# Optimization experiments

Measured on AMD Instinct MI355X. Metric: run time of the kernel, lower is better.

Reference implementation:

```python
import jax, jax.numpy as jnp
import numpy as np


def gru_step(x, h, Wih, Whh, bih, bhh):
    gi = x @ Wih.T + bih            # [N, 3H]
    gh = h @ Whh.T + bhh            # [N, 3H]
    ir, iz, inn = jnp.split(gi, 3, axis=-1)
    hr, hz, hn = jnp.split(gh, 3, axis=-1)
    r = jax.nn.sigmoid(ir + hr)
    z = jax.nn.sigmoid(iz + hz)
    n = jnp.tanh(inn + r * hn)
    return (1.0 - z) * n + z * h


def setup_inputs() -> dict:
    key = jax.random.key(0)
    ks = jax.random.split(key, 24)
    B, T, X, HE, HC = 8192, 30, 64, 256, 32
    s = 0.05
    rn = lambda k, shp: (jax.random.normal(k, shp, dtype=jnp.float32) * s)
    return {
        "batch_features": jax.random.normal(ks[0], (B, 2, T, X), dtype=jnp.float32),
        "coords": jax.random.uniform(ks[1], (B, T, 4), dtype=jnp.float32) * 100.0,
        "valid_mask": jax.random.bernoulli(ks[2], 0.8, (B, T)),
        # Event GRU (2 layers, input 64, hidden 256)
        "Wih0": rn(ks[3], (3 * HE, X)),  "Whh0": rn(ks[4], (3 * HE, HE)),
        "bih0": jnp.zeros((3 * HE,), jnp.float32), "bhh0": jnp.zeros((3 * HE,), jnp.float32),
        "Wih1": rn(ks[5], (3 * HE, HE)), "Whh1": rn(ks[6], (3 * HE, HE)),
        "bih1": jnp.zeros((3 * HE,), jnp.float32), "bhh1": jnp.zeros((3 * HE,), jnp.float32),
        # Coord GRU (1 layer, input 4, hidden 32)
        "WihC": rn(ks[7], (3 * HC, 4)), "WhhC": rn(ks[8], (3 * HC, HC)),
        "bihC": jnp.zeros((3 * HC,), jnp.float32), "bhhC": jnp.zeros((3 * HC,), jnp.float32),
        # Fusion module
        "We": rn(ks[9], (128, HE)), "be": jnp.zeros((128,), jnp.float32),
        "Wc": rn(ks[10], (128, HC)), "bc": jnp.zeros((128,), jnp.float32),
        "W1": rn(ks[11], (128, 256)), "b1": jnp.zeros((128,), jnp.float32),
        "W2": rn(ks[12], (2, 128)), "b2": jnp.zeros((2,), jnp.float32),
    }


def reference(batch_features, coords, valid_mask,
              Wih0, Whh0, bih0, bhh0, Wih1, Whh1, bih1, bhh1,
              WihC, WhhC, bihC, bhhC,
              We, be, Wc, bc, W1, b1, W2, b2):
    B, F, T, X = batch_features.shape  # F == 2 frames
    N = B * T
    HE = Whh0.shape[1]
    HC = WhhC.shape[1]
    # [B,2,T,X] -> [N,2,X]: per-track (prev, curr) feature sequence
    feats = jnp.transpose(batch_features, (0, 2, 1, 3)).reshape(N, F, X)
    h0 = jnp.zeros((N, HE), batch_features.dtype)
    h1 = jnp.zeros((N, HE), batch_features.dtype)
    for t in range(F):  # fixed 2-step unroll (n_frames=2)
        h0 = gru_step(feats[:, t], h0, Wih0, Whh0, bih0, bhh0)
        h1 = gru_step(h0, h1, Wih1, Whh1, bih1, bhh1)
    event_out = h1  # [N, 256] (dropout between GRU layers inactive in eval)
    # coord GRU: single step from zero state
    c = coords.reshape(N, 4)
    coord_out = gru_step(c, jnp.zeros((N, HC), coords.dtype), WihC, WhhC, bihC, bhhC)
    # fusion
    ep = event_out @ We.T + be          # [N,128]
    cp = coord_out @ Wc.T + bc          # [N,128]
    hid = jax.nn.relu(jnp.concatenate([ep, cp], axis=-1) @ W1.T + b1)
    logits = hid @ W2.T + b2            # [N,2]
    logits = logits.reshape(B, T, 2)
    # invalid tracks were skipped in the original; mask them to zero here
    return jnp.where(valid_mask[..., None], logits, 0.0)
```

## Files before the change

### kernel.cpp

```cpp
#include <hip/hip_runtime.h>


#define NROWS 245760
#define TT 30
#define KC 64

typedef __attribute__((ext_vector_type(4))) float f32x4;
typedef __attribute__((ext_vector_type(8))) short bf16x8;
typedef __attribute__((ext_vector_type(4))) int i32x4;

__device__ __forceinline__ float bf2f(unsigned short u) {
    union { unsigned int u; float f; } v; v.u = ((unsigned int)u) << 16; return v.f;
}
__device__ __forceinline__ unsigned short f2bf(float f) {
    union { float f; unsigned int u; } v; v.f = f;
    unsigned int u = v.u;
    unsigned int r = u + 0x7fffu + ((u >> 16) & 1u);
    return (unsigned short)(r >> 16);
}
__device__ __forceinline__ float fexp2c(float x) {
    return __builtin_amdgcn_exp2f(fminf(x, 80.f));
}
__device__ __forceinline__ float fsigmoid(float x) {
    return __builtin_amdgcn_rcpf(1.f + fexp2c(-1.44269504f * x));
}
__device__ __forceinline__ float ftanh(float x) {
    float t = fexp2c(-2.88539008f * x);
    return (1.f - t) * __builtin_amdgcn_rcpf(1.f + t);
}
__device__ __forceinline__ f32x4 mfma16(bf16x8 a, bf16x8 b, f32x4 c) {
    return __builtin_amdgcn_mfma_f32_16x16x32_bf16(a, b, c, 0, 0, 0);
}


__global__ void cvt_bf16(const float* __restrict__ src, unsigned short* __restrict__ dst, int n) {
    int i = blockIdx.x * 256 + threadIdx.x;
    if (i < n) dst[i] = f2bf(src[i]);
}

__global__ void bias_prep(const float* __restrict__ bih0, const float* __restrict__ bhh0, float* __restrict__ BC0,
                          const float* __restrict__ bih1, const float* __restrict__ bhh1, float* __restrict__ BC1) {
    int j = threadIdx.x;
    BC0[j]       = bih0[j]       + bhh0[j];
    BC0[256 + j] = bih0[256 + j] + bhh0[256 + j];
    BC0[512 + j] = bih0[512 + j];
    BC0[768 + j] = bhh0[512 + j];
    BC1[j]       = bih1[j]       + bhh1[j];
    BC1[256 + j] = bih1[256 + j] + bhh1[256 + j];
    BC1[512 + j] = bih1[512 + j];
    BC1[768 + j] = bhh1[512 + j];
}

__global__ void fuse_prep(const float* __restrict__ We, const float* __restrict__ be,
                          const float* __restrict__ Wc, const float* __restrict__ bc_,
                          const float* __restrict__ W1, const float* __restrict__ b1,
                          unsigned short* __restrict__ WF, float* __restrict__ BF) {
    int idx = blockIdx.x * 256 + threadIdx.x;
    if (idx >= 128 * 320) return;
    int o = idx / 320, k = idx - o * 320;
    float v = 0.f;
    if (k < 256) {
        for (int i = 0; i < 128; ++i) v += W1[o * 256 + i] * We[i * 256 + k];
    } else if (k < 288) {
        int kk = k - 256;
        for (int i = 0; i < 128; ++i) v += W1[o * 256 + 128 + i] * Wc[i * 32 + kk];
    }
    WF[o * 320 + k] = f2bf(v);
    if (k == 0) {
        float s = b1[o];
        for (int i = 0; i < 128; ++i) s += W1[o * 256 + i] * be[i];
        for (int i = 0; i < 128; ++i) s += W1[o * 256 + 128 + i] * bc_[i];
        BF[o] = s;
    }
}

__global__ void xprep(const float* __restrict__ bf, unsigned short* __restrict__ A1,
                      unsigned short* __restrict__ A3) {
    int i = blockIdx.x * 256 + threadIdx.x;
    int n = i >> 6, k = i & 63;
    int b = n / TT, t = n - b * TT;
    const float* p = bf + ((size_t)(b * 2) * TT + t) * 64 + k;
    A1[(size_t)n * 64 + k]  = f2bf(p[0]);
    A3[(size_t)n * 320 + k] = f2bf(p[TT * 64]);
}

__global__ void coord_gru(const float* __restrict__ coords, const float* __restrict__ WihC,
                          const float* __restrict__ bihC, const float* __restrict__ bhhC,
                          unsigned short* __restrict__ A5) {
    int n = blockIdx.x * 256 + threadIdx.x;
    if (n >= NROWS) return;
    const float4 c = *(const float4*)(coords + (size_t)n * 4);
    unsigned short* o = A5 + (size_t)n * 320 + 256;
    for (int j = 0; j < 32; ++j) {
        float gr = WihC[j * 4 + 0] * c.x + WihC[j * 4 + 1] * c.y + WihC[j * 4 + 2] * c.z + WihC[j * 4 + 3] * c.w + bihC[j];
        int j2 = 32 + j;
        float gz = WihC[j2 * 4 + 0] * c.x + WihC[j2 * 4 + 1] * c.y + WihC[j2 * 4 + 2] * c.z + WihC[j2 * 4 + 3] * c.w + bihC[j2];
        int j3 = 64 + j;
        float gn = WihC[j3 * 4 + 0] * c.x + WihC[j3 * 4 + 1] * c.y + WihC[j3 * 4 + 2] * c.z + WihC[j3 * 4 + 3] * c.w + bihC[j3];
        float r = fsigmoid(gr + bhhC[j]);
        float z = fsigmoid(gz + bhhC[j2]);
        float nn = ftanh(gn + r * bhhC[j3]);
        o[j] = f2bf((1.f - z) * nn);
    }
    for (int j = 32; j < 64; ++j) o[j] = 0;
}

__device__ __forceinline__ void gemm_phase(
    const unsigned short* __restrict__ Ag, int lda, int aoff, int Kp,
    const unsigned short* __restrict__ Wg,
    unsigned short* sA, unsigned short* sW,
    int row0, int cb, int tid,
    f32x4 (&aR)[2][4], f32x4 (&aZ)[2][4], f32x4 (&aG)[2][4]) {
    const int lane = tid & 63, wave = tid >> 6;
    const int lr = lane & 15, lk = lane >> 4;
    const int xr = (lr & 7) * 8;
    for (int kc = 0; kc < Kp; kc += KC) {
        __syncthreads();
#pragma unroll
        for (int it = 0; it < 4; ++it) {
            int tau = tid + it * 256;
            int r = tau >> 3, g = tau & 7;
            i32x4 v = *(const i32x4*)(Ag + (size_t)(row0 + r) * lda + aoff + kc + g * 8);
            *(i32x4*)(sA + r * KC + ((g * 8) ^ ((r & 7) * 8))) = v;
        }
#pragma unroll
        for (int it = 0; it < 6; ++it) {
            int tau = tid + it * 256;
            int wr = tau >> 3, g = tau & 7;
            int t = wr >> 4, c = wr & 15;
            int grow = (t >> 2) * 256 + cb * 64 + (t & 3) * 16 + c;
            i32x4 v = *(const i32x4*)(Wg + (size_t)grow * Kp + kc + g * 8);
            *(i32x4*)(sW + wr * KC + ((g * 8) ^ ((wr & 7) * 8))) = v;
        }
        __syncthreads();
#pragma unroll
        for (int kk = 0; kk < 2; ++kk) {
            int kx = (kk * 32 + lk * 8) ^ xr;
            bf16x8 a0 = *(const bf16x8*)(sA + (wave * 32 + lr) * KC + kx);
            bf16x8 a1 = *(const bf16x8*)(sA + (wave * 32 + 16 + lr) * KC + kx);
#pragma unroll
            for (int t = 0; t < 12; ++t) {
                bf16x8 b = *(const bf16x8*)(sW + (t * 16 + lr) * KC + kx);
                int gi = t & 3;
                if (t < 4) {
                    aR[0][gi] = mfma16(a0, b, aR[0][gi]);
                    aR[1][gi] = mfma16(a1, b, aR[1][gi]);
                } else if (t < 8) {
                    aZ[0][gi] = mfma16(a0, b, aZ[0][gi]);
                    aZ[1][gi] = mfma16(a1, b, aZ[1][gi]);
                } else {
                    aG[0][gi] = mfma16(a0, b, aG[0][gi]);
                    aG[1][gi] = mfma16(a1, b, aG[1][gi]);
                }
            }
        }
    }
}

template <bool HAS_HH, bool HAS_HPREV>
__global__ __launch_bounds__(256, 2) void gru_gemm(
    const unsigned short* __restrict__ A, int lda,
    int Kih, const unsigned short* __restrict__ Wih,
    int Khh, const unsigned short* __restrict__ Whh,
    const float* __restrict__ bc,
    const unsigned short* __restrict__ hprev, int ldh,
    unsigned short* __restrict__ dst, int ldd) {
    __shared__ unsigned short sA[128 * KC];
    __shared__ unsigned short sW[192 * KC];
    const int tid = threadIdx.x;
    const int row0 = blockIdx.x * 128;
    const int cb = blockIdx.y;
    f32x4 aR[2][4] = {}, aZ[2][4] = {}, aIN[2][4] = {}, aHN[2][4] = {};
    gemm_phase(A, lda, 0, Kih, Wih, sA, sW, row0, cb, tid, aR, aZ, aIN);
    if (HAS_HH)
        gemm_phase(A, lda, Kih, Khh, Whh, sA, sW, row0, cb, tid, aR, aZ, aHN);
    const int lane = tid & 63, wave = tid >> 6;
    const int lr = lane & 15, lk = lane >> 4;
    const int jc = cb * 64;
    const int rb = row0 + wave * 32;
#pragma unroll
    for (int s = 0; s < 2; ++s) {
#pragma unroll
        for (int gi = 0; gi < 4; ++gi) {
            int j = jc + gi * 16 + lr;
            float br = bc[j], bz = bc[256 + j], bin = bc[512 + j], bhn = bc[768 + j];
#pragma unroll
            for (int q = 0; q < 4; ++q) {
                int row = rb + s * 16 + lk * 4 + q;
                float rg = fsigmoid(aR[s][gi][q] + br);
                float zg = fsigmoid(aZ[s][gi][q] + bz);
                float hn = HAS_HH ? aHN[s][gi][q] : 0.f;
                float ng = ftanh(aIN[s][gi][q] + bin + rg * (hn + bhn));
                float h = (1.f - zg) * ng;
                if (HAS_HPREV) h += zg * bf2f(hprev[(size_t)row * ldh + j]);
                dst[(size_t)row * ldd + j] = f2bf(h);
            }
        }
    }
}

__global__ __launch_bounds__(256, 2) void fusion_logits(
    const unsigned short* __restrict__ A,
    const unsigned short* __restrict__ WF,
    const float* __restrict__ BF, const float* __restrict__ W2, const float* __restrict__ b2,
    const int* __restrict__ mask, float* __restrict__ out) {
    __shared__ unsigned short sA[64 * KC];
    __shared__ unsigned short sW[128 * KC];
    const int tid = threadIdx.x, lane = tid & 63, wave = tid >> 6;
    const int lr = lane & 15, lk = lane >> 4;
    const int xr = (lr & 7) * 8;
    const int row0 = blockIdx.x * 64;
    f32x4 acc[8] = {};
    for (int kc = 0; kc < 320; kc += KC) {
        __syncthreads();
#pragma unroll
        for (int it = 0; it < 2; ++it) {
            int tau = tid + it * 256;
            int r = tau >> 3, g = tau & 7;
            i32x4 v = *(const i32x4*)(A + (size_t)(row0 + r) * 320 + kc + g * 8);
            *(i32x4*)(sA + r * KC + ((g * 8) ^ ((r & 7) * 8))) = v;
        }
#pragma unroll
        for (int it = 0; it < 4; ++it) {
            int tau = tid + it * 256;
            int wr = tau >> 3, g = tau & 7;
            i32x4 v = *(const i32x4*)(WF + (size_t)wr * 320 + kc + g * 8);
            *(i32x4*)(sW + wr * KC + ((g * 8) ^ ((wr & 7) * 8))) = v;
        }
        __syncthreads();
#pragma unroll
        for (int kk = 0; kk < 2; ++kk) {
            int kx = (kk * 32 + lk * 8) ^ xr;
            bf16x8 a = *(const bf16x8*)(sA + (wave * 16 + lr) * KC + kx);
#pragma unroll
            for (int t = 0; t < 8; ++t) {
                bf16x8 b = *(const bf16x8*)(sW + (t * 16 + lr) * KC + kx);
                acc[t] = mfma16(a, b, acc[t]);
            }
        }
    }
#pragma unroll
    for (int q = 0; q < 4; ++q) {
        float l0 = 0.f, l1 = 0.f;
#pragma unroll
        for (int t = 0; t < 8; ++t) {
            int j = t * 16 + lr;
            float h = acc[t][q] + BF[j];
            h = h > 0.f ? h : 0.f;
            l0 += h * W2[j];
            l1 += h * W2[128 + j];
        }
#pragma unroll
        for (int m = 1; m < 16; m <<= 1) {
            l0 += __shfl_xor(l0, m, 64);
            l1 += __shfl_xor(l1, m, 64);
        }
        if (lr == 0) {
            int row = row0 + wave * 16 + lk * 4 + q;
            float v0 = l0 + b2[0], v1 = l1 + b2[1];
            if (!mask[row]) { v0 = 0.f; v1 = 0.f; }
            out[(size_t)row * 2]     = v0;
            out[(size_t)row * 2 + 1] = v1;
        }
    }
}


extern "C" void kernel_launch(void* const* d_in, const int* in_sizes, int n_in,
                              void* d_out, int out_size, void* d_ws, size_t ws_size,
                              hipStream_t stream) {
    const float* bfeat  = (const float*)d_in[0];
    const float* coords = (const float*)d_in[1];
    const int* mask = (const int*)d_in[2];
    const float* Wih0 = (const float*)d_in[3];
    const float* Whh0 = (const float*)d_in[4];
    const float* bih0 = (const float*)d_in[5];
    const float* bhh0 = (const float*)d_in[6];
    const float* Wih1 = (const float*)d_in[7];
    const float* Whh1 = (const float*)d_in[8];
    const float* bih1 = (const float*)d_in[9];
    const float* bhh1 = (const float*)d_in[10];
    const float* WihC = (const float*)d_in[11];
    const float* bihC = (const float*)d_in[13];
    const float* bhhC = (const float*)d_in[14];
    const float* We = (const float*)d_in[15];
    const float* be = (const float*)d_in[16];
    const float* Wc = (const float*)d_in[17];
    const float* bc_ = (const float*)d_in[18];
    const float* W1 = (const float*)d_in[19];
    const float* b1 = (const float*)d_in[20];
    const float* W2 = (const float*)d_in[21];
    const float* b2 = (const float*)d_in[22];
    float* out = (float*)d_out;

    const size_t N = NROWS;
    char* ws = (char*)d_ws;
    unsigned short* A4 = (unsigned short*)ws;
    unsigned short* A1 = (unsigned short*)ws;
    unsigned short* A3 = (unsigned short*)(ws + N * 512 * 2);
    unsigned short* A5 = A3;
    char* wp = ws + N * 512 * 2 + N * 320 * 2;
    unsigned short* WB0  = (unsigned short*)wp; wp += 768 * 64 * 2;
    unsigned short* WBh0 = (unsigned short*)wp; wp += 768 * 256 * 2;
    unsigned short* WB1  = (unsigned short*)wp; wp += 768 * 256 * 2;
    unsigned short* WBh1 = (unsigned short*)wp; wp += 768 * 256 * 2;
    unsigned short* WF   = (unsigned short*)wp; wp += 128 * 320 * 2;
    float* BC0 = (float*)wp; wp += 1024 * 4;
    float* BC1 = (float*)wp; wp += 1024 * 4;
    float* BF  = (float*)wp; wp += 128 * 4;

    cvt_bf16<<<192, 256, 0, stream>>>(Wih0, WB0, 768 * 64);
    cvt_bf16<<<768, 256, 0, stream>>>(Whh0, WBh0, 768 * 256);
    cvt_bf16<<<768, 256, 0, stream>>>(Wih1, WB1, 768 * 256);
    cvt_bf16<<<768, 256, 0, stream>>>(Whh1, WBh1, 768 * 256);
    bias_prep<<<1, 256, 0, stream>>>(bih0, bhh0, BC0, bih1, bhh1, BC1);
    fuse_prep<<<160, 256, 0, stream>>>(We, be, Wc, bc_, W1, b1, WF, BF);
    xprep<<<61440, 256, 0, stream>>>(bfeat, A1, A3);

    dim3 gg(NROWS / 128, 4);
    gru_gemm<false, false><<<gg, 256, 0, stream>>>(A1, 64, 64, WB0, 0, nullptr, BC0, nullptr, 0, A3 + 64, 320);
    gru_gemm<false, false><<<gg, 256, 0, stream>>>(A3 + 64, 320, 256, WB1, 0, nullptr, BC1, nullptr, 0, A4 + 256, 512);
    gru_gemm<true, true><<<gg, 256, 0, stream>>>(A3, 320, 64, WB0, 256, WBh0, BC0, A3 + 64, 320, A4, 512);
    coord_gru<<<NROWS / 256, 256, 0, stream>>>(coords, WihC, bihC, bhhC, A5);
    gru_gemm<true, true><<<gg, 256, 0, stream>>>(A4, 512, 256, WB1, 256, WBh1, BC1, A4 + 256, 512, A5, 320);
    fusion_logits<<<NROWS / 64, 256, 0, stream>>>(A5, WF, BF, W2, b2, mask, out);

    (void)in_sizes; (void)n_in; (void)out_size; (void)ws_size;
}
```

Before: 950.0 us.

## Load GEMM tiles directly into LDS and remap workgroups across XCDs

Replaces the register-staged global-to-LDS copies in the GRU GEMM and fusion kernels with global_load_lds 16-byte direct loads. The XOR swizzle moves from the LDS write address to the global source column. It also flattens the 2D grid and remaps block IDs so the four column blocks sharing a row tile run on the same XCD, which should improve L2 reuse of the A rows. The occupancy hint is raised to three blocks per CU, which may add register pressure or spills.

```diff
diff --git a/kernel.cpp b/kernel.cpp
--- a/kernel.cpp
+++ b/kernel.cpp
@@ -7,7 +7,6 @@
 
 typedef __attribute__((ext_vector_type(4))) float f32x4;
 typedef __attribute__((ext_vector_type(8))) short bf16x8;
-typedef __attribute__((ext_vector_type(4))) int i32x4;
 
 __device__ __forceinline__ float bf2f(unsigned short u) {
     union { unsigned int u; float f; } v; v.u = ((unsigned int)u) << 16; return v.f;
@@ -30,6 +29,11 @@
 }
 __device__ __forceinline__ f32x4 mfma16(bf16x8 a, bf16x8 b, f32x4 c) {
     return __builtin_amdgcn_mfma_f32_16x16x32_bf16(a, b, c, 0, 0, 0);
+}
+__device__ __forceinline__ void gload16(const unsigned short* g, unsigned short* l) {
+    __builtin_amdgcn_global_load_lds(
+        (const __attribute__((address_space(1))) void*)g,
+        (__attribute__((address_space(3))) void*)l, 16, 0, 0);
 }
 
 
@@ -114,23 +118,24 @@
     const int lane = tid & 63, wave = tid >> 6;
     const int lr = lane & 15, lk = lane >> 4;
     const int xr = (lr & 7) * 8;
+    const int gsrc = ((lane & 7) ^ (lane >> 3)) * 8;
+    const int lrow = lane >> 3;
     for (int kc = 0; kc < Kp; kc += KC) {
         __syncthreads();
 #pragma unroll
         for (int it = 0; it < 4; ++it) {
-            int tau = tid + it * 256;
-            int r = tau >> 3, g = tau & 7;
-            i32x4 v = *(const i32x4*)(Ag + (size_t)(row0 + r) * lda + aoff + kc + g * 8);
-            *(i32x4*)(sA + r * KC + ((g * 8) ^ ((r & 7) * 8))) = v;
+            int grp = it * 4 + wave;
+            const unsigned short* src = Ag + (size_t)(row0 + grp * 8 + lrow) * lda + aoff + kc + gsrc;
+            gload16(src, sA + grp * 512);
         }
 #pragma unroll
         for (int it = 0; it < 6; ++it) {
-            int tau = tid + it * 256;
-            int wr = tau >> 3, g = tau & 7;
-            int t = wr >> 4, c = wr & 15;
+            int gw = it * 4 + wave;
+            int t = gw >> 1;
+            int c = (gw & 1) * 8 + lrow;
             int grow = (t >> 2) * 256 + cb * 64 + (t & 3) * 16 + c;
-            i32x4 v = *(const i32x4*)(Wg + (size_t)grow * Kp + kc + g * 8);
-            *(i32x4*)(sW + wr * KC + ((g * 8) ^ ((wr & 7) * 8))) = v;
+            const unsigned short* src = Wg + (size_t)grow * Kp + kc + gsrc;
+            gload16(src, sW + gw * 512);
         }
         __syncthreads();
 #pragma unroll
@@ -158,7 +163,7 @@
 }
 
 template <bool HAS_HH, bool HAS_HPREV>
-__global__ __launch_bounds__(256, 2) void gru_gemm(
+__global__ __launch_bounds__(256, 3) void gru_gemm(
     const unsigned short* __restrict__ A, int lda,
     int Kih, const unsigned short* __restrict__ Wih,
     int Khh, const unsigned short* __restrict__ Whh,
@@ -168,8 +173,10 @@
     __shared__ unsigned short sA[128 * KC];
     __shared__ unsigned short sW[192 * KC];
     const int tid = threadIdx.x;
-    const int row0 = blockIdx.x * 128;
-    const int cb = blockIdx.y;
+    const int nwg = gridDim.x;
+    const int wgid = (blockIdx.x & 7) * (nwg >> 3) + (blockIdx.x >> 3);
+    const int cb = wgid & 3;
+    const int row0 = (wgid >> 2) * 128;
     f32x4 aR[2][4] = {}, aZ[2][4] = {}, aIN[2][4] = {}, aHN[2][4] = {};
     gemm_phase(A, lda, 0, Kih, Wih, sA, sW, row0, cb, tid, aR, aZ, aIN);
     if (HAS_HH)
@@ -199,7 +206,7 @@
     }
 }
 
-__global__ __launch_bounds__(256, 2) void fusion_logits(
+__global__ __launch_bounds__(256, 3) void fusion_logits(
     const unsigned short* __restrict__ A,
     const unsigned short* __restrict__ WF,
     const float* __restrict__ BF, const float* __restrict__ W2, const float* __restrict__ b2,
@@ -209,23 +216,23 @@
     const int tid = threadIdx.x, lane = tid & 63, wave = tid >> 6;
     const int lr = lane & 15, lk = lane >> 4;
     const int xr = (lr & 7) * 8;
+    const int gsrc = ((lane & 7) ^ (lane >> 3)) * 8;
+    const int lrow = lane >> 3;
     const int row0 = blockIdx.x * 64;
     f32x4 acc[8] = {};
     for (int kc = 0; kc < 320; kc += KC) {
         __syncthreads();
 #pragma unroll
         for (int it = 0; it < 2; ++it) {
-            int tau = tid + it * 256;
-            int r = tau >> 3, g = tau & 7;
-            i32x4 v = *(const i32x4*)(A + (size_t)(row0 + r) * 320 + kc + g * 8);
-            *(i32x4*)(sA + r * KC + ((g * 8) ^ ((r & 7) * 8))) = v;
+            int grp = it * 4 + wave;
+            const unsigned short* src = A + (size_t)(row0 + grp * 8 + lrow) * 320 + kc + gsrc;
+            gload16(src, sA + grp * 512);
         }
 #pragma unroll
         for (int it = 0; it < 4; ++it) {
-            int tau = tid + it * 256;
-            int wr = tau >> 3, g = tau & 7;
-            i32x4 v = *(const i32x4*)(WF + (size_t)wr * 320 + kc + g * 8);
-            *(i32x4*)(sW + wr * KC + ((g * 8) ^ ((wr & 7) * 8))) = v;
+            int gw = it * 4 + wave;
+            const unsigned short* src = WF + (size_t)(gw * 8 + lrow) * 320 + kc + gsrc;
+            gload16(src, sW + gw * 512);
         }
         __syncthreads();
 #pragma unroll
@@ -317,7 +324,7 @@
     fuse_prep<<<160, 256, 0, stream>>>(We, be, Wc, bc_, W1, b1, WF, BF);
     xprep<<<61440, 256, 0, stream>>>(bfeat, A1, A3);
 
-    dim3 gg(NROWS / 128, 4);
+    const int gg = (NROWS / 128) * 4;
     gru_gemm<false, false><<<gg, 256, 0, stream>>>(A1, 64, 64, WB0, 0, nullptr, BC0, nullptr, 0, A3 + 64, 320);
     gru_gemm<false, false><<<gg, 256, 0, stream>>>(A3 + 64, 320, 256, WB1, 0, nullptr, BC1, nullptr, 0, A4 + 256, 512);
     gru_gemm<true, true><<<gg, 256, 0, stream>>>(A3, 320, 64, WB0, 256, WBh0, BC0, A3 + 64, 320, A4, 512);
```

Result: faster. 791.0 us (-16.7%).
